# Kernel optimization log

Hardware: AMD Instinct MI355X
Metric: run time of the kernel (lower is better)

Reference implementation:

```python
import jax, jax.numpy as jnp
import numpy as np

N = 16384; T = 65536; H = 128; G = 512; E = 65536; NEI = 32768
NIT = 4  # num_interactions
NL = 4   # finaldepth (hidden layers after the first)
EPS = 1e-5
INV = float(1.0 / np.sqrt(1.0 + EPS))  # fresh BatchNorm1d in eval mode: running_mean=0, running_var=1


def _bn(x, g, b):
    # eval-mode BatchNorm with mean=0, var=1: (x - 0)/sqrt(1+eps)*gamma + beta
    return x * (g * INV) + b


def setup_inputs() -> dict:
    key = jax.random.key(0)
    ks = jax.random.split(key, 16)
    inp = {}
    inp["node_positions"] = jax.random.normal(ks[0], (N, 2), jnp.float32)
    inp["edge_index_2rd"] = jax.random.randint(ks[1], (3, T), 0, N)  # (i, j, k) triplets
    inp["edx_jk"] = jax.random.randint(ks[2], (T,), 0, E)
    inp["edx_ij"] = jax.random.randint(ks[3], (T,), 0, E)
    inp["num_edge_inside"] = NEI
    inp["node_to_feature"] = jax.random.randint(ks[4], (N,), 0, G)
    # mlp_geo: Linear(3, H) + BN
    inp["Wg"] = jax.random.normal(ks[5], (3, H), jnp.float32) / np.sqrt(3.0)
    inp["bg"] = jnp.zeros((H,), jnp.float32)
    inp["gamg"] = 1.0 + 0.1 * jax.random.normal(ks[6], (H,), jnp.float32)
    inp["betg"] = 0.1 * jax.random.normal(ks[7], (H,), jnp.float32)
    # per-interaction (NIT), per-edge-type-group (4) MLPs
    inp["W0"] = jax.random.normal(ks[8], (NIT, 4, 4 * H, H), jnp.float32) / np.sqrt(4.0 * H)
    inp["b0"] = jnp.zeros((NIT, 4, H), jnp.float32)
    inp["g0"] = 1.0 + 0.1 * jax.random.normal(ks[9], (NIT, 4, H), jnp.float32)
    inp["be0"] = 0.1 * jax.random.normal(ks[10], (NIT, 4, H), jnp.float32)
    inp["Wh"] = jax.random.normal(ks[11], (NIT, NL, 4, H, H), jnp.float32) / np.sqrt(float(H))
    inp["bh"] = jnp.zeros((NIT, NL, 4, H), jnp.float32)
    inp["gh"] = 1.0 + 0.1 * jax.random.normal(ks[12], (NIT, NL, 4, H), jnp.float32)
    inp["beh"] = 0.1 * jax.random.normal(ks[13], (NIT, NL, 4, H), jnp.float32)
    inp["att"] = jnp.ones((4,), jnp.float32)
    return inp


def reference(node_positions, Wg, bg, gamg, betg, W0, b0, g0, be0, Wh, bh, gh, beh, att,
              edge_index_2rd, edx_jk, edx_ij, num_edge_inside, node_to_feature):
    i, j, k = edge_index_2rd[0], edge_index_2rd[1], edge_index_2rd[2]
    # geometric features of each triplet (i<-j<-k)
    v1 = node_positions[j] - node_positions[i]   # [T,2]
    v2 = node_positions[k] - node_positions[j]   # [T,2]
    d_ij = jnp.linalg.norm(v1, axis=1)
    d_jk = jnp.linalg.norm(v2, axis=1)
    cross = v1[:, 0] * v2[:, 1] - v1[:, 1] * v2[:, 0]
    dot = jnp.sum(v1 * v2, axis=1)
    theta = jnp.arctan2(jnp.abs(cross), dot)
    geo = jnp.stack([d_ij, d_jk, theta], axis=-1)        # [T,3]
    geo = jax.nn.relu(_bn(geo @ Wg + bg, gamg, betg))    # [T,H] geo_encoding

    # 4 mutually exclusive edge-type masks
    in1 = edx_ij < num_edge_inside
    in2 = edx_jk < num_edge_inside
    masks = jnp.stack([in1 & in2, in1 & ~in2, ~in1 & in2, ~in1 & ~in2], axis=0)  # [4,T]
    mask_f = masks.astype(geo.dtype)[:, :, None]         # [4,T,1]

    num_nodes = node_positions.shape[0]
    nf = jnp.zeros((num_nodes, H), geo.dtype)            # input_feature = zeros
    outs = []
    for it in range(NIT):
        x = jnp.concatenate([nf[i], nf[j], nf[k], geo], axis=-1)  # [T,4H]
        h = jnp.einsum('ti,gio->gto', x, W0[it]) + b0[it][:, None, :]
        h = jax.nn.relu(_bn(h, g0[it][:, None, :], be0[it][:, None, :]))
        for l in range(NL):
            h = jnp.einsum('gti,gio->gto', h, Wh[it, l]) + bh[it, l][:, None, :]
            h = jax.nn.relu(_bn(h, gh[it, l][:, None, :], beh[it, l][:, None, :]))
        h = jax.nn.leaky_relu(h, 0.01) * att[:, None, None]       # [4,T,H]
        x_out = jnp.sum(h * mask_f, axis=0)                       # disjoint masks -> select
        nf = jax.ops.segment_sum(x_out, i, num_segments=num_nodes)  # scatter_add over i
        outs.append(nf)
    out = jnp.concatenate(outs, axis=1)                           # [N, NIT*H]
    emb = jax.ops.segment_sum(out, node_to_feature, num_segments=G)  # global_add_pool
    return jnp.minimum(emb, 1.0e6)
```

## Files before the change

### kernel.cpp

```cpp
#include <hip/hip_runtime.h>
#include <hip/hip_bf16.h>
#include <math.h>

#define N_NODES 16384
#define T_TRI   65536
#define H_DIM   128
#define G_POOL  512
#define NITER   4
#define NLAY    4
#define RMAX    (T_TRI + 512)
#define MT      (RMAX / 128)

#define INV_STD 0.9999950000374996f

typedef __attribute__((ext_vector_type(8))) short bhalf8;
typedef __attribute__((ext_vector_type(4))) float f32x4;

__device__ __forceinline__ unsigned short f2b(float f) {
    unsigned int u = __float_as_uint(f);
    unsigned int r = (u + 0x7fffu + ((u >> 16) & 1u)) >> 16;
    return (unsigned short)r;
}
__device__ __forceinline__ float b2f(unsigned short b) {
    return __uint_as_float(((unsigned int)b) << 16);
}


__device__ __forceinline__ int group_of(int eij, int ejk, int nei) {
    return ((eij < nei) ? 0 : 2) + ((ejk < nei) ? 0 : 1);
}

__global__ void histboth_k(const int* __restrict__ edxjk, const int* __restrict__ edxij,
                           const int* __restrict__ neip, const int* __restrict__ eidx,
                           int* __restrict__ ints, int* __restrict__ cnt) {
    __shared__ int lc[4];
    if (threadIdx.x < 4) lc[threadIdx.x] = 0;
    __syncthreads();
    int t = blockIdx.x * 256 + threadIdx.x;
    int nei = *neip;
    int g = group_of(edxij[t], edxjk[t], nei);
    atomicAdd(&lc[g], 1);
    atomicAdd(&cnt[eidx[t]], 1);
    __syncthreads();
    if (threadIdx.x < 4) atomicAdd(&ints[threadIdx.x], lc[threadIdx.x]);
}

__global__ void scanoff_k(int* __restrict__ ints, int* __restrict__ cnt,
                          int* __restrict__ row_start) {
    __shared__ int part[256];
    int tid = threadIdx.x;
    if (tid == 0) {
        int a = 0;
        ints[8] = 0;
        for (int g = 0; g < 4; ++g) {
            a = (a + ints[g] + 127) & ~127;
            ints[9 + g] = a;
        }
    }
    int base = tid * 64;
    int s = 0;
    for (int q = 0; q < 64; ++q) s += cnt[base + q];
    part[tid] = s;
    __syncthreads();
    if (tid == 0) {
        int run = 0;
        for (int q = 0; q < 256; ++q) { int v = part[q]; part[q] = run; run += v; }
        row_start[N_NODES] = run;
    }
    __syncthreads();
    int p = part[tid];
    for (int q = 0; q < 64; ++q) {
        int c = cnt[base + q];
        row_start[base + q] = p;
        cnt[base + q] = p;
        p += c;
    }
}

__global__ void scatboth_k(const int* __restrict__ edxjk, const int* __restrict__ edxij,
                           const int* __restrict__ neip, const int* __restrict__ eidx,
                           int* __restrict__ ints, int* __restrict__ rowmap,
                           int* __restrict__ cursor, int* __restrict__ row_ids) {
    int t = blockIdx.x * 256 + threadIdx.x;
    int nei = *neip;
    int g = group_of(edxij[t], edxjk[t], nei);
    int lane = threadIdx.x & 63;
    unsigned long long msame = 0;
    #pragma unroll
    for (int q = 0; q < 4; ++q) {
        unsigned long long mq = __ballot(g == q);
        if (g == q) msame = mq;
    }
    int leader = __ffsll((long long)msame) - 1;
    int rank = __popcll(msame & ((1ull << lane) - 1ull));
    int base = 0;
    if (lane == leader) base = atomicAdd(&ints[4 + g], __popcll(msame));
    base = __shfl(base, leader);
    int pos = ints[8 + g] + base + rank;
    rowmap[pos] = t;
    int slot = atomicAdd(&cursor[eidx[t]], 1);
    row_ids[slot] = pos;
}


__global__ void t0_k(const float* __restrict__ W0, unsigned short* __restrict__ WT0) {
    __shared__ float t[32][33];
    int b = blockIdx.x;
    int ig = b >> 6;
    int kt = (b >> 2) & 15;
    int nt = b & 3;
    int tx = threadIdx.x & 31, ty = threadIdx.x >> 5;
    const float* src = W0 + ((size_t)ig * 512 + kt * 32) * 128 + nt * 32;
    #pragma unroll
    for (int q = 0; q < 4; ++q) { int r = q * 8 + ty; t[r][tx] = src[(size_t)r * 128 + tx]; }
    __syncthreads();
    unsigned short* dst = WT0 + ((size_t)ig * 128 + nt * 32) * 512 + kt * 32;
    #pragma unroll
    for (int q = 0; q < 4; ++q) { int r = q * 8 + ty; dst[(size_t)r * 512 + tx] = f2b(t[tx][r]); }
}

__global__ void th_k(const float* __restrict__ Wh, unsigned short* __restrict__ WTh) {
    __shared__ float t[32][33];
    int b = blockIdx.x;
    int ilg = b >> 4;
    int kt = (b >> 2) & 3;
    int nt = b & 3;
    int tx = threadIdx.x & 31, ty = threadIdx.x >> 5;
    const float* src = Wh + ((size_t)ilg * 128 + kt * 32) * 128 + nt * 32;
    #pragma unroll
    for (int q = 0; q < 4; ++q) { int r = q * 8 + ty; t[r][tx] = src[(size_t)r * 128 + tx]; }
    __syncthreads();
    unsigned short* dst = WTh + ((size_t)ilg * 128 + nt * 32) * 128 + kt * 32;
    #pragma unroll
    for (int q = 0; q < 4; ++q) { int r = q * 8 + ty; dst[(size_t)r * 128 + tx] = f2b(t[tx][r]); }
}


__global__ void geo_k(const float* __restrict__ pos, const int* __restrict__ eidx,
                      const float* __restrict__ Wg, const float* __restrict__ bg,
                      const float* __restrict__ gamg, const float* __restrict__ betg,
                      unsigned short* __restrict__ geob) {
    int t = blockIdx.x * 2 + (threadIdx.x >> 7);
    int h = threadIdx.x & 127;
    int ni = eidx[t], nj = eidx[T_TRI + t], nk = eidx[2 * T_TRI + t];
    float ix = pos[2 * ni], iy = pos[2 * ni + 1];
    float jx = pos[2 * nj], jy = pos[2 * nj + 1];
    float kx = pos[2 * nk], ky = pos[2 * nk + 1];
    float v1x = jx - ix, v1y = jy - iy;
    float v2x = kx - jx, v2y = ky - jy;
    float dij = sqrtf(v1x * v1x + v1y * v1y);
    float djk = sqrtf(v2x * v2x + v2y * v2y);
    float cr = v1x * v2y - v1y * v2x;
    float dt = v1x * v2x + v1y * v2y;
    float th = atan2f(fabsf(cr), dt);
    float v = dij * Wg[h] + djk * Wg[128 + h] + th * Wg[256 + h] + bg[h];
    v = v * (gamg[h] * INV_STD) + betg[h];
    v = fmaxf(v, 0.0f);
    geob[(size_t)t * 128 + h] = f2b(v);
}


template<int SKIPNF>
__global__ __launch_bounds__(256, 2) void chain_k(
    const unsigned short* __restrict__ nfb, const unsigned short* __restrict__ geob,
    const int* __restrict__ eidx, const int* __restrict__ rowmap,
    const int* __restrict__ aoff, const unsigned short* __restrict__ WT0,
    const float* __restrict__ b0, const float* __restrict__ g0, const float* __restrict__ be0,
    const unsigned short* __restrict__ WTh,
    const float* __restrict__ bhp, const float* __restrict__ ghp, const float* __restrict__ behp,
    const float* __restrict__ att, unsigned short* __restrict__ hfinal,
    int it) {
    __shared__ unsigned short sh[128 * 128];
    __shared__ unsigned short sw[128 * 128];
    unsigned short* As = sw;
    unsigned short* Bs = sw + 128 * 64;

    const int r0 = blockIdx.x * 128;
    int g = 0;
    if (r0 >= aoff[1]) g = 1;
    if (r0 >= aoff[2]) g = 2;
    if (r0 >= aoff[3]) g = 3;
    const int tid = threadIdx.x;
    const int lane = tid & 63;
    const int wid = tid >> 6;
    const int wm = wid >> 1, wn = wid & 1;
    const int lr = lane & 15, lq = lane >> 4;

    const int myrow = tid >> 3;
    const int mycolb = (tid & 7) * 8;
    int ttv[4], offi[4], offj[4], offk2[4], offt[4];
    #pragma unroll
    for (int p = 0; p < 4; ++p) {
        int row = p * 32 + myrow;
        int tt = rowmap[r0 + row];
        ttv[p] = tt;
        int ts = tt < 0 ? 0 : tt;
        offt[p] = ts * 128;
        if (!SKIPNF) {
            offi[p]  = eidx[ts] * 128;
            offj[p]  = eidx[T_TRI + ts] * 128;
            offk2[p] = eidx[2 * T_TRI + ts] * 128;
        }
    }

    f32x4 acc[4][4];
    const f32x4 zero4 = {0.f, 0.f, 0.f, 0.f};
    #pragma unroll
    for (int m = 0; m < 4; ++m)
        #pragma unroll
        for (int n = 0; n < 4; ++n) acc[m][n] = zero4;

    const unsigned short* Wt = WT0 + (size_t)(it * 4 + g) * 128 * 512;
    #pragma unroll
    for (int k0 = (SKIPNF ? 384 : 0); k0 < 512; k0 += 64) {
        const int region = k0 >> 7;
        const int half = k0 & 127;
        #pragma unroll
        for (int p = 0; p < 4; ++p) {
            int row = p * 32 + myrow;
            int4 v = {0, 0, 0, 0};
            if (ttv[p] >= 0) {
                const unsigned short* src =
                    region == 0 ? nfb + offi[p] :
                    region == 1 ? nfb + offj[p] :
                    region == 2 ? nfb + offk2[p] :
                                  geob + offt[p];
                v = *reinterpret_cast<const int4*>(src + half + mycolb);
            }
            *reinterpret_cast<int4*>(&As[row * 64 + (((tid & 7) ^ (row & 7)) << 3)]) = v;
        }
        #pragma unroll
        for (int p = 0; p < 4; ++p) {
            int n = p * 32 + myrow;
            int4 v = *reinterpret_cast<const int4*>(Wt + (size_t)n * 512 + k0 + mycolb);
            *reinterpret_cast<int4*>(&Bs[n * 64 + (((tid & 7) ^ (n & 7)) << 3)]) = v;
        }
        __syncthreads();
        #pragma unroll
        for (int ks = 0; ks < 2; ++ks) {
            bhalf8 af[4], bf[4];
            #pragma unroll
            for (int m = 0; m < 4; ++m) {
                int row = 64 * wm + 16 * m + lr;
                int c8 = (4 * ks + lq) ^ (row & 7);
                af[m] = *reinterpret_cast<const bhalf8*>(&As[row * 64 + (c8 << 3)]);
            }
            #pragma unroll
            for (int n = 0; n < 4; ++n) {
                int nn = 64 * wn + 16 * n + lr;
                int c8 = (4 * ks + lq) ^ (nn & 7);
                bf[n] = *reinterpret_cast<const bhalf8*>(&Bs[nn * 64 + (c8 << 3)]);
            }
            #pragma unroll
            for (int m = 0; m < 4; ++m)
                #pragma unroll
                for (int n = 0; n < 4; ++n)
                    acc[m][n] = __builtin_amdgcn_mfma_f32_16x16x32_bf16(af[m], bf[n], acc[m][n], 0, 0, 0);
        }
        __syncthreads();
    }

    int4 wreg[8];
    {
        const unsigned short* Wl = WTh + (size_t)((it * NLAY + 0) * 4 + g) * 128 * 128;
        #pragma unroll
        for (int p = 0; p < 8; ++p) {
            int idx = p * 256 + tid;
            int n = idx >> 4, gd = idx & 15;
            wreg[p] = *reinterpret_cast<const int4*>(Wl + n * 128 + ((gd ^ (n & 7)) << 3));
        }
    }
    {
        const float* bb = b0 + (it * 4 + g) * 128;
        const float* gg = g0 + (it * 4 + g) * 128;
        const float* be = be0 + (it * 4 + g) * 128;
        #pragma unroll
        for (int n = 0; n < 4; ++n) {
            int col = 64 * wn + 16 * n + lr;
            float sc = gg[col] * INV_STD;
            float bbc = bb[col], bec = be[col];
            int gc = col >> 3, cl = col & 7;
            #pragma unroll
            for (int m = 0; m < 4; ++m)
                #pragma unroll
                for (int r = 0; r < 4; ++r) {
                    int row = 64 * wm + 16 * m + 4 * lq + r;
                    float v = fmaxf((acc[m][n][r] + bbc) * sc + bec, 0.0f);
                    sh[row * 128 + ((gc ^ (row & 7)) << 3) + cl] = f2b(v);
                }
        }
    }
    #pragma unroll
    for (int p = 0; p < 8; ++p) {
        int idx = p * 256 + tid;
        *reinterpret_cast<int4*>(&sw[idx * 8]) = wreg[p];
    }
    __syncthreads();

    for (int l = 0; l < NLAY; ++l) {
        if (l + 1 < NLAY) {
            const unsigned short* Wn = WTh + (size_t)((it * NLAY + l + 1) * 4 + g) * 128 * 128;
            #pragma unroll
            for (int p = 0; p < 8; ++p) {
                int idx = p * 256 + tid;
                int n = idx >> 4, gd = idx & 15;
                wreg[p] = *reinterpret_cast<const int4*>(Wn + n * 128 + ((gd ^ (n & 7)) << 3));
            }
        }
        #pragma unroll
        for (int m = 0; m < 4; ++m)
            #pragma unroll
            for (int n = 0; n < 4; ++n) acc[m][n] = zero4;
        #pragma unroll
        for (int kk = 0; kk < 4; ++kk) {
            bhalf8 af[4], bf[4];
            #pragma unroll
            for (int m = 0; m < 4; ++m) {
                int row = 64 * wm + 16 * m + lr;
                int gc = (4 * kk + lq) ^ (row & 7);
                af[m] = *reinterpret_cast<const bhalf8*>(&sh[row * 128 + (gc << 3)]);
            }
            #pragma unroll
            for (int n = 0; n < 4; ++n) {
                int nn = 64 * wn + 16 * n + lr;
                int gc = (4 * kk + lq) ^ (nn & 7);
                bf[n] = *reinterpret_cast<const bhalf8*>(&sw[nn * 128 + (gc << 3)]);
            }
            #pragma unroll
            for (int m = 0; m < 4; ++m)
                #pragma unroll
                for (int n = 0; n < 4; ++n)
                    acc[m][n] = __builtin_amdgcn_mfma_f32_16x16x32_bf16(af[m], bf[n], acc[m][n], 0, 0, 0);
        }
        if (l + 1 < NLAY) {
            __syncthreads();
            const int ilg = (it * NLAY + l) * 4 + g;
            const float* bb = bhp + (size_t)ilg * 128;
            const float* gg = ghp + (size_t)ilg * 128;
            const float* be = behp + (size_t)ilg * 128;
            #pragma unroll
            for (int n = 0; n < 4; ++n) {
                int col = 64 * wn + 16 * n + lr;
                float sc = gg[col] * INV_STD;
                float bbc = bb[col], bec = be[col];
                int gc = col >> 3, cl = col & 7;
                #pragma unroll
                for (int m = 0; m < 4; ++m)
                    #pragma unroll
                    for (int r = 0; r < 4; ++r) {
                        int row = 64 * wm + 16 * m + 4 * lq + r;
                        float v = fmaxf((acc[m][n][r] + bbc) * sc + bec, 0.0f);
                        sh[row * 128 + ((gc ^ (row & 7)) << 3) + cl] = f2b(v);
                    }
            }
            #pragma unroll
            for (int p = 0; p < 8; ++p) {
                int idx = p * 256 + tid;
                *reinterpret_cast<int4*>(&sw[idx * 8]) = wreg[p];
            }
            __syncthreads();
        }
    }

    {
        const int ilg = (it * NLAY + (NLAY - 1)) * 4 + g;
        const float* bb = bhp + (size_t)ilg * 128;
        const float* gg = ghp + (size_t)ilg * 128;
        const float* be = behp + (size_t)ilg * 128;
        float attg = att[g];
        #pragma unroll
        for (int n = 0; n < 4; ++n) {
            int col = 64 * wn + 16 * n + lr;
            float sc = gg[col] * INV_STD;
            float bbc = bb[col], bec = be[col];
            #pragma unroll
            for (int m = 0; m < 4; ++m)
                #pragma unroll
                for (int r = 0; r < 4; ++r) {
                    int row = r0 + 64 * wm + 16 * m + 4 * lq + r;
                    float v = fmaxf((acc[m][n][r] + bbc) * sc + bec, 0.0f) * attg;
                    hfinal[(size_t)row * 128 + col] = f2b(v);
                }
        }
    }
}


__global__ void reduce_k(const unsigned short* __restrict__ hfinal,
                         const int* __restrict__ row_start, const int* __restrict__ row_ids,
                         const int* __restrict__ ntf, unsigned short* __restrict__ nfb,
                         float* __restrict__ emb, int itoff) {
    int n = blockIdx.x * 2 + (threadIdx.x >> 7);
    int c = threadIdx.x & 127;
    int s = row_start[n], e = row_start[n + 1];
    float acc = 0.0f;
    for (int r = s; r < e; ++r) {
        int rid = row_ids[r];
        acc += b2f(hfinal[(size_t)rid * 128 + c]);
    }
    nfb[(size_t)n * 128 + c] = f2b(acc);
    atomicAdd(&emb[(size_t)ntf[n] * 512 + itoff + c], acc);
}

__global__ void clamp_k(const float* __restrict__ emb, float* __restrict__ out) {
    int i = blockIdx.x * 256 + threadIdx.x;
    out[i] = fminf(emb[i], 1.0e6f);
}


extern "C" void kernel_launch(void* const* d_in, const int* in_sizes, int n_in,
                              void* d_out, int out_size, void* d_ws, size_t ws_size,
                              hipStream_t stream) {
    (void)in_sizes; (void)n_in; (void)out_size; (void)ws_size;
    const float* pos   = (const float*)d_in[0];
    const int*   eidx  = (const int*)d_in[1];
    const int*   edxjk = (const int*)d_in[2];
    const int*   edxij = (const int*)d_in[3];
    const int*   neip  = (const int*)d_in[4];
    const int*   ntf   = (const int*)d_in[5];
    const float* Wg    = (const float*)d_in[6];
    const float* bg    = (const float*)d_in[7];
    const float* gamg  = (const float*)d_in[8];
    const float* betg  = (const float*)d_in[9];
    const float* W0    = (const float*)d_in[10];
    const float* b0    = (const float*)d_in[11];
    const float* g0    = (const float*)d_in[12];
    const float* be0   = (const float*)d_in[13];
    const float* Wh    = (const float*)d_in[14];
    const float* bhp   = (const float*)d_in[15];
    const float* ghp   = (const float*)d_in[16];
    const float* behp  = (const float*)d_in[17];
    const float* att   = (const float*)d_in[18];

    char* w = (char*)d_ws;
    size_t off = 0;
    auto alloc = [&](size_t b) -> char* {
        char* p = w + off;
        off += (b + 255) & ~(size_t)255;
        return p;
    };
    int* ints            = (int*)alloc(256);
    int* rowmap          = (int*)alloc((size_t)RMAX * 4);
    int* cnt             = (int*)alloc((size_t)N_NODES * 4);
    int* row_start       = (int*)alloc((size_t)(N_NODES + 1) * 4);
    int* row_ids         = (int*)alloc((size_t)T_TRI * 4);
    unsigned short* WT0  = (unsigned short*)alloc((size_t)16 * 128 * 512 * 2);
    unsigned short* WTh  = (unsigned short*)alloc((size_t)64 * 128 * 128 * 2);
    unsigned short* geob = (unsigned short*)alloc((size_t)T_TRI * 128 * 2);
    unsigned short* nfb  = (unsigned short*)alloc((size_t)N_NODES * 128 * 2);
    unsigned short* hfin = (unsigned short*)alloc((size_t)RMAX * 128 * 2);
    float* emb           = (float*)alloc((size_t)G_POOL * 512 * 4);

    hipMemsetAsync(ints, 0, 256, stream);
    hipMemsetAsync(rowmap, 0xFF, (size_t)RMAX * 4, stream);
    hipMemsetAsync(cnt, 0, (size_t)N_NODES * 4, stream);
    hipMemsetAsync(emb, 0, (size_t)G_POOL * 512 * 4, stream);

    histboth_k<<<256, 256, 0, stream>>>(edxjk, edxij, neip, eidx, ints, cnt);
    scanoff_k<<<1, 256, 0, stream>>>(ints, cnt, row_start);
    scatboth_k<<<256, 256, 0, stream>>>(edxjk, edxij, neip, eidx, ints, rowmap, cnt, row_ids);
    t0_k<<<1024, 256, 0, stream>>>(W0, WT0);
    th_k<<<1024, 256, 0, stream>>>(Wh, WTh);
    geo_k<<<T_TRI / 2, 256, 0, stream>>>(pos, eidx, Wg, bg, gamg, betg, geob);

    for (int it = 0; it < NITER; ++it) {
        if (it == 0)
            chain_k<1><<<MT, 256, 0, stream>>>(nfb, geob, eidx, rowmap, ints + 8, WT0, b0, g0, be0,
                                               WTh, bhp, ghp, behp, att, hfin, it);
        else
            chain_k<0><<<MT, 256, 0, stream>>>(nfb, geob, eidx, rowmap, ints + 8, WT0, b0, g0, be0,
                                               WTh, bhp, ghp, behp, att, hfin, it);
        reduce_k<<<N_NODES / 2, 256, 0, stream>>>(hfin, row_start, row_ids, ntf, nfb, emb, it * 128);
    }

    clamp_k<<<1024, 256, 0, stream>>>(emb, (float*)d_out);
}
```

Measured before the change: 524.3 us.

## Double-buffer first-layer GEMM loads and vectorize geo and hfinal stores

The first-layer K loop now prefetches the next A/B tiles into registers while MFMAs run on the current LDS buffer. The two LDS arrays (sw and sh) serve as ping-pong buffers, which leaves one barrier per step instead of two. The final hfinal output is staged through swizzled LDS and written as coalesced 16-byte rows rather than scattered 2-byte stores. geo_k now computes 8 channels per thread and writes them with one int4 store, which cuts redundant triplet geometry work. The cost is higher register pressure from the prefetch registers and extra barriers in the epilogue.

```diff
diff --git a/kernel.cpp b/kernel.cpp
--- a/kernel.cpp
+++ b/kernel.cpp
@@ -140,8 +140,8 @@
                       const float* __restrict__ Wg, const float* __restrict__ bg,
                       const float* __restrict__ gamg, const float* __restrict__ betg,
                       unsigned short* __restrict__ geob) {
-    int t = blockIdx.x * 2 + (threadIdx.x >> 7);
-    int h = threadIdx.x & 127;
+    int t = blockIdx.x * 16 + (threadIdx.x >> 4);
+    int h0 = (threadIdx.x & 15) * 8;
     int ni = eidx[t], nj = eidx[T_TRI + t], nk = eidx[2 * T_TRI + t];
     float ix = pos[2 * ni], iy = pos[2 * ni + 1];
     float jx = pos[2 * nj], jy = pos[2 * nj + 1];
@@ -153,10 +153,22 @@
     float cr = v1x * v2y - v1y * v2x;
     float dt = v1x * v2x + v1y * v2y;
     float th = atan2f(fabsf(cr), dt);
-    float v = dij * Wg[h] + djk * Wg[128 + h] + th * Wg[256 + h] + bg[h];
-    v = v * (gamg[h] * INV_STD) + betg[h];
-    v = fmaxf(v, 0.0f);
-    geob[(size_t)t * 128 + h] = f2b(v);
+    unsigned int ov[4];
+    #pragma unroll
+    for (int q = 0; q < 4; ++q) {
+        unsigned int lo, hi;
+        #pragma unroll
+        for (int e = 0; e < 2; ++e) {
+            int h = h0 + q * 2 + e;
+            float v = dij * Wg[h] + djk * Wg[128 + h] + th * Wg[256 + h] + bg[h];
+            v = v * (gamg[h] * INV_STD) + betg[h];
+            v = fmaxf(v, 0.0f);
+            if (e == 0) lo = f2b(v); else hi = f2b(v);
+        }
+        ov[q] = lo | (hi << 16);
+    }
+    int4 o = { (int)ov[0], (int)ov[1], (int)ov[2], (int)ov[3] };
+    *reinterpret_cast<int4*>(&geob[(size_t)t * 128 + h0]) = o;
 }
 
 
@@ -172,8 +184,6 @@
     int it) {
     __shared__ unsigned short sh[128 * 128];
     __shared__ unsigned short sw[128 * 128];
-    unsigned short* As = sw;
-    unsigned short* Bs = sw + 128 * 64;
 
     const int r0 = blockIdx.x * 128;
     int g = 0;
@@ -211,13 +221,16 @@
         for (int n = 0; n < 4; ++n) acc[m][n] = zero4;
 
     const unsigned short* Wt = WT0 + (size_t)(it * 4 + g) * 128 * 512;
-    #pragma unroll
-    for (int k0 = (SKIPNF ? 384 : 0); k0 < 512; k0 += 64) {
-        const int region = k0 >> 7;
-        const int half = k0 & 127;
+    constexpr int KSTEPS = SKIPNF ? 2 : 8;
+    constexpr int KBASE  = SKIPNF ? 384 : 0;
+    unsigned short* bufs[2] = { sw, sh };
+    int4 ra[4], rb[4];
+
+    {
+        const int k0 = KBASE;
+        const int region = k0 >> 7, half = k0 & 127;
         #pragma unroll
         for (int p = 0; p < 4; ++p) {
-            int row = p * 32 + myrow;
             int4 v = {0, 0, 0, 0};
             if (ttv[p] >= 0) {
                 const unsigned short* src =
@@ -227,15 +240,42 @@
                                   geob + offt[p];
                 v = *reinterpret_cast<const int4*>(src + half + mycolb);
             }
-            *reinterpret_cast<int4*>(&As[row * 64 + (((tid & 7) ^ (row & 7)) << 3)]) = v;
+            ra[p] = v;
+            rb[p] = *reinterpret_cast<const int4*>(Wt + (size_t)(p * 32 + myrow) * 512 + k0 + mycolb);
         }
         #pragma unroll
         for (int p = 0; p < 4; ++p) {
-            int n = p * 32 + myrow;
-            int4 v = *reinterpret_cast<const int4*>(Wt + (size_t)n * 512 + k0 + mycolb);
-            *reinterpret_cast<int4*>(&Bs[n * 64 + (((tid & 7) ^ (n & 7)) << 3)]) = v;
+            int row = p * 32 + myrow;
+            int sz = (((tid & 7) ^ (row & 7)) << 3);
+            *reinterpret_cast<int4*>(&bufs[0][row * 64 + sz]) = ra[p];
+            *reinterpret_cast<int4*>(&bufs[0][128 * 64 + row * 64 + sz]) = rb[p];
         }
         __syncthreads();
+    }
+
+    #pragma unroll
+    for (int s = 0; s < KSTEPS; ++s) {
+        const int cur = s & 1;
+        if (s + 1 < KSTEPS) {
+            const int k1 = KBASE + (s + 1) * 64;
+            const int region = k1 >> 7, half = k1 & 127;
+            #pragma unroll
+            for (int p = 0; p < 4; ++p) {
+                int4 v = {0, 0, 0, 0};
+                if (ttv[p] >= 0) {
+                    const unsigned short* src =
+                        region == 0 ? nfb + offi[p] :
+                        region == 1 ? nfb + offj[p] :
+                        region == 2 ? nfb + offk2[p] :
+                                      geob + offt[p];
+                    v = *reinterpret_cast<const int4*>(src + half + mycolb);
+                }
+                ra[p] = v;
+                rb[p] = *reinterpret_cast<const int4*>(Wt + (size_t)(p * 32 + myrow) * 512 + k1 + mycolb);
+            }
+        }
+        const unsigned short* Ab = bufs[cur];
+        const unsigned short* Bb = bufs[cur] + 128 * 64;
         #pragma unroll
         for (int ks = 0; ks < 2; ++ks) {
             bhalf8 af[4], bf[4];
@@ -243,19 +283,29 @@
             for (int m = 0; m < 4; ++m) {
                 int row = 64 * wm + 16 * m + lr;
                 int c8 = (4 * ks + lq) ^ (row & 7);
-                af[m] = *reinterpret_cast<const bhalf8*>(&As[row * 64 + (c8 << 3)]);
+                af[m] = *reinterpret_cast<const bhalf8*>(&Ab[row * 64 + (c8 << 3)]);
             }
             #pragma unroll
             for (int n = 0; n < 4; ++n) {
                 int nn = 64 * wn + 16 * n + lr;
                 int c8 = (4 * ks + lq) ^ (nn & 7);
-                bf[n] = *reinterpret_cast<const bhalf8*>(&Bs[nn * 64 + (c8 << 3)]);
+                bf[n] = *reinterpret_cast<const bhalf8*>(&Bb[nn * 64 + (c8 << 3)]);
             }
             #pragma unroll
             for (int m = 0; m < 4; ++m)
                 #pragma unroll
                 for (int n = 0; n < 4; ++n)
                     acc[m][n] = __builtin_amdgcn_mfma_f32_16x16x32_bf16(af[m], bf[n], acc[m][n], 0, 0, 0);
+        }
+        if (s + 1 < KSTEPS) {
+            unsigned short* An = bufs[cur ^ 1];
+            #pragma unroll
+            for (int p = 0; p < 4; ++p) {
+                int row = p * 32 + myrow;
+                int sz = (((tid & 7) ^ (row & 7)) << 3);
+                *reinterpret_cast<int4*>(&An[row * 64 + sz]) = ra[p];
+                *reinterpret_cast<int4*>(&An[128 * 64 + row * 64 + sz]) = rb[p];
+            }
         }
         __syncthreads();
     }
@@ -362,6 +412,7 @@
         }
     }
 
+    __syncthreads();
     {
         const int ilg = (it * NLAY + (NLAY - 1)) * 4 + g;
         const float* bb = bhp + (size_t)ilg * 128;
@@ -373,15 +424,24 @@
             int col = 64 * wn + 16 * n + lr;
             float sc = gg[col] * INV_STD;
             float bbc = bb[col], bec = be[col];
+            int gc = col >> 3, cl = col & 7;
             #pragma unroll
             for (int m = 0; m < 4; ++m)
                 #pragma unroll
                 for (int r = 0; r < 4; ++r) {
-                    int row = r0 + 64 * wm + 16 * m + 4 * lq + r;
+                    int row = 64 * wm + 16 * m + 4 * lq + r;
                     float v = fmaxf((acc[m][n][r] + bbc) * sc + bec, 0.0f) * attg;
-                    hfinal[(size_t)row * 128 + col] = f2b(v);
+                    sh[row * 128 + ((gc ^ (row & 7)) << 3) + cl] = f2b(v);
                 }
         }
+    }
+    __syncthreads();
+    #pragma unroll
+    for (int p = 0; p < 8; ++p) {
+        int idx = p * 256 + tid;
+        int row = idx >> 4, gd = idx & 15;
+        int4 v = *reinterpret_cast<const int4*>(&sh[row * 128 + ((gd ^ (row & 7)) << 3)]);
+        *reinterpret_cast<int4*>(&hfinal[(size_t)(r0 + row) * 128 + gd * 8]) = v;
     }
 }
 
@@ -461,7 +521,7 @@
     scatboth_k<<<256, 256, 0, stream>>>(edxjk, edxij, neip, eidx, ints, rowmap, cnt, row_ids);
     t0_k<<<1024, 256, 0, stream>>>(W0, WT0);
     th_k<<<1024, 256, 0, stream>>>(Wh, WTh);
-    geo_k<<<T_TRI / 2, 256, 0, stream>>>(pos, eidx, Wg, bg, gamg, betg, geob);
+    geo_k<<<T_TRI / 16, 256, 0, stream>>>(pos, eidx, Wg, bg, gamg, betg, geob);
 
     for (int it = 0; it < NITER; ++it) {
         if (it == 0)
```

Measured after the change: 488.5 us. 1.07x faster.
